# Kernel tuning notes

Hardware: AMD Instinct MI355X
Metric: run time of the kernel (lower is better)

The kernel has to match this reference:

```python
import jax, jax.numpy as jnp
import numpy as np

RADIUS = 3
TEMP = 0.1
EPS = 1e-6


def bilinear_resize(x, oh, ow):
    # Matches torch F.interpolate(mode='bilinear', align_corners=False):
    # half-pixel centers, source coord clamped to >= 0, no antialiasing.
    b, c, h, w = x.shape
    ys = jnp.maximum((jnp.arange(oh, dtype=x.dtype) + 0.5) * (h / oh) - 0.5, 0.0)
    xs = jnp.maximum((jnp.arange(ow, dtype=x.dtype) + 0.5) * (w / ow) - 0.5, 0.0)
    y0f = jnp.floor(ys)
    x0f = jnp.floor(xs)
    wy = (ys - y0f)[:, None]          # [oh,1]
    wx = (xs - x0f)[None, :]          # [1,ow]
    y0 = jnp.clip(y0f, 0, h - 1).astype(jnp.int32)
    y1 = jnp.clip(y0f + 1, 0, h - 1).astype(jnp.int32)
    x0 = jnp.clip(x0f, 0, w - 1).astype(jnp.int32)
    x1 = jnp.clip(x0f + 1, 0, w - 1).astype(jnp.int32)
    r0 = x[:, :, y0, :]
    r1 = x[:, :, y1, :]
    v00 = r0[:, :, :, x0]; v01 = r0[:, :, :, x1]
    v10 = r1[:, :, :, x0]; v11 = r1[:, :, :, x1]
    return (1 - wy) * ((1 - wx) * v00 + wx * v01) + wy * ((1 - wx) * v10 + wx * v11)


def setup_inputs() -> dict:
    key = jax.random.key(0)
    k1, k2, k3 = jax.random.split(key, 3)
    fL = jax.random.normal(k1, (4, 256, 96, 320), dtype=jnp.float32)
    fR = jax.random.normal(k2, (4, 256, 96, 320), dtype=jnp.float32)
    disp_full = jax.random.uniform(k3, (4, 1, 384, 1280), dtype=jnp.float32) * 64.0
    return {"fL": fL, "fR": fR, "disp_full": disp_full}


def reference(fL, fR, disp_full):
    B, C, h4, w4 = fL.shape
    H, W = disp_full.shape[-2], disp_full.shape[-1]
    # quarter-res disparity
    disp0 = bilinear_resize(disp_full, h4, w4) / 4.0            # [B,1,h4,w4]
    # cosine correlation volume over 2*radius+1 horizontal shifts
    nL = fL / jnp.clip(jnp.linalg.norm(fL, axis=1, keepdims=True), EPS)
    nR = fR / jnp.clip(jnp.linalg.norm(fR, axis=1, keepdims=True), EPS)
    sims = [jnp.sum(nL * jnp.roll(nR, d, axis=-1), axis=1)
            for d in range(-RADIUS, RADIUS + 1)]
    # original wraps build_cosine_cost in @torch.no_grad()
    cost = jax.lax.stop_gradient(jnp.stack(sims, axis=1))       # [B,7,h4,w4]
    p = jax.nn.softmax(cost / TEMP, axis=1)
    offsets = jnp.arange(-RADIUS, RADIUS + 1, dtype=fL.dtype).reshape(1, -1, 1, 1)
    delta = jnp.sum(p * offsets, axis=1, keepdims=True)          # [B,1,h4,w4]
    disp_ref = disp0 + delta
    conf = jnp.max(p, axis=1, keepdims=True)
    # laplacian smoothing (smooth=True)
    lap = jnp.array([[0., 1., 0.], [1., -4., 1.], [0., 1., 0.]], dtype=fL.dtype).reshape(1, 1, 3, 3)
    lap_out = jax.lax.conv_general_dilated(disp_ref, lap, (1, 1), [(1, 1), (1, 1)])
    disp_q = disp_ref - 0.2 * lap_out
    disp_full_ref = bilinear_resize(disp_q, H, W) * 4.0
    conf_full = bilinear_resize(conf, H, W)
    return disp_full_ref, conf_full
```

## Files before the change

### kernel.cpp

```cpp
#include <hip/hip_runtime.h>
#include <math.h>

constexpr int B_ = 4, C_ = 256, H4 = 96, W4 = 320, HF = 384, WF = 1280;
constexpr int CHUNKS = 5;
constexpr float EPSV = 1e-6f;
constexpr int LOW = B_ * H4 * W4;
constexpr int FULL = B_ * HF * WF;

__global__ __launch_bounds__(256)
void phase1(const float* __restrict__ fL, const float* __restrict__ fR,
            const float* __restrict__ D, float* __restrict__ dref,
            float* __restrict__ conf)
{
    const int bi = blockIdx.x;
    const int chunk = bi % CHUNKS;
    const int y = (bi / CHUNKS) % H4;
    const int b = bi / (CHUNKS * H4);
    const int tid = threadIdx.x;
    const int wave = tid >> 6;
    const int lane = tid & 63;
    const int x0 = chunk * 64;
    const int x = x0 + lane;

    const size_t chanStride = (size_t)H4 * W4;
    const size_t rowBase = (((size_t)b * C_) * H4 + y) * W4;

    int hx = x, hslot = 0;
    const bool isHalo = (lane < 6);
    if (lane < 3)      { hx = x0 - 3 + lane;        if (hx < 0)   hx += W4; hslot = lane; }
    else if (lane < 6) { hx = x0 + 64 + (lane - 3); if (hx >= W4) hx -= W4; hslot = 64 + lane; }

    float dot[7] = {0.f,0.f,0.f,0.f,0.f,0.f,0.f};
    float ssL = 0.f, ssR = 0.f, ssH = 0.f;

    __shared__ float4 stage4[4][72];
    float4* const sw = stage4[wave];

    const float* pLb = fL + rowBase + (size_t)(wave * 64) * chanStride;
    const float* pRb = fR + rowBase + (size_t)(wave * 64) * chanStride;

    float aa[4], rr[4], hh[4];
    size_t off = 0;
#pragma unroll
    for (int j = 0; j < 4; ++j) {
        aa[j] = pLb[off + x]; rr[j] = pRb[off + x]; hh[j] = pRb[off + hx];
        off += chanStride;
    }

#pragma unroll 4
    for (int it = 0; it < 16; ++it) {
        const float ca0 = aa[0], ca1 = aa[1], ca2 = aa[2], ca3 = aa[3];
        const float4 rq = make_float4(rr[0], rr[1], rr[2], rr[3]);
        const float4 hq = make_float4(hh[0], hh[1], hh[2], hh[3]);

        sw[3 + lane] = rq;
        if (isHalo) sw[hslot] = hq;

        if (it < 15) {
#pragma unroll
            for (int j = 0; j < 4; ++j) {
                aa[j] = pLb[off + x]; rr[j] = pRb[off + x]; hh[j] = pRb[off + hx];
                off += chanStride;
            }
        }

        __builtin_amdgcn_s_waitcnt(0xC07F);

#pragma unroll
        for (int k = 0; k < 7; ++k) {
            const float4 t = sw[lane + k];
            dot[k] += ca0 * t.x + ca1 * t.y + ca2 * t.z + ca3 * t.w;
        }
        ssL += ca0 * ca0 + ca1 * ca1 + ca2 * ca2 + ca3 * ca3;
        ssR += rq.x * rq.x + rq.y * rq.y + rq.z * rq.z + rq.w * rq.w;
        ssH += hq.x * hq.x + hq.y * hq.y + hq.z * hq.z + hq.w * hq.w;
    }

    __shared__ float part[256][11];
    __shared__ float sss[70];
#pragma unroll
    for (int k = 0; k < 7; ++k) part[tid][k] = dot[k];
    part[tid][7] = ssL;
    part[tid][8] = ssR;
    part[tid][9] = ssH;
    __syncthreads();

    float rdot[7], rssL = 0.f;
    if (tid < 64) {
#pragma unroll
        for (int k = 0; k < 7; ++k)
            rdot[k] = part[tid][k] + part[tid + 64][k] + part[tid + 128][k] + part[tid + 192][k];
        rssL = part[tid][7] + part[tid + 64][7] + part[tid + 128][7] + part[tid + 192][7];
        float rssR = part[tid][8] + part[tid + 64][8] + part[tid + 128][8] + part[tid + 192][8];
        sss[3 + tid] = rssR;
        if (tid < 6) {
            float hh2 = part[tid][9] + part[tid + 64][9] + part[tid + 128][9] + part[tid + 192][9];
            if (tid < 3) sss[tid] = hh2;
            else         sss[64 + tid] = hh2;
        }
    }
    __syncthreads();

    if (tid < 64) {
        const float nL = fmaxf(sqrtf(rssL), EPSV);
        float cost[7];
#pragma unroll
        for (int k = 0; k < 7; ++k) {
            float nR = fmaxf(sqrtf(sss[tid + k]), EPSV);
            float s = rdot[k] / (nL * nR);
            cost[6 - k] = s * 10.0f;
        }
        float m = cost[0];
#pragma unroll
        for (int i = 1; i < 7; ++i) m = fmaxf(m, cost[i]);
        float sum = 0.f, dsum = 0.f;
#pragma unroll
        for (int i = 0; i < 7; ++i) {
            float e = __expf(cost[i] - m);
            sum += e;
            dsum += e * (float)(i - 3);
        }
        const float delta = dsum / sum;
        const float cf = 1.0f / sum;

        const int xpix = x0 + tid;
        const int Y0 = 4 * y + 1, X0 = 4 * xpix + 1;
        const size_t dbase = ((size_t)b * HF + Y0) * WF + X0;
        const float s4 = D[dbase] + D[dbase + 1] + D[dbase + WF] + D[dbase + WF + 1];
        const float disp0 = s4 * 0.0625f;

        const size_t o = ((size_t)b * H4 + y) * W4 + xpix;
        dref[o] = disp0 + delta;
        conf[o] = cf;
    }
}

__device__ __forceinline__ float dq_val(const float* __restrict__ dref,
                                        size_t base, int yq, int xq)
{
    size_t i = base + (size_t)yq * W4 + xq;
    float c  = dref[i];
    float up = (yq > 0)      ? dref[i - W4] : 0.f;
    float dn = (yq < H4 - 1) ? dref[i + W4] : 0.f;
    float lf = (xq > 0)      ? dref[i - 1]  : 0.f;
    float rt = (xq < W4 - 1) ? dref[i + 1]  : 0.f;
    return c - 0.2f * (up + dn + lf + rt - 4.f * c);
}

__global__ void phase2(const float* __restrict__ dref, const float* __restrict__ cf,
                       float* __restrict__ out)
{
    int i = blockIdx.x * blockDim.x + threadIdx.x;
    if (i >= FULL) return;
    int X = i % WF;
    int Y = (i / WF) % HF;
    int b = i / (WF * HF);
    float ys = fmaxf((Y + 0.5f) * 0.25f - 0.5f, 0.f);
    float xs = fmaxf((X + 0.5f) * 0.25f - 0.5f, 0.f);
    float y0f = floorf(ys), x0f = floorf(xs);
    float wy = ys - y0f, wx = xs - x0f;
    int y0 = min((int)y0f, H4 - 1);
    int x0 = min((int)x0f, W4 - 1);
    int y1 = min(y0 + 1, H4 - 1);
    int x1 = min(x0 + 1, W4 - 1);
    size_t base = (size_t)b * (H4 * W4);

    float d = (1.f - wy) * ((1.f - wx) * dq_val(dref, base, y0, x0) + wx * dq_val(dref, base, y0, x1))
            +        wy  * ((1.f - wx) * dq_val(dref, base, y1, x0) + wx * dq_val(dref, base, y1, x1));

    size_t i00 = base + (size_t)y0 * W4 + x0;
    size_t i01 = base + (size_t)y0 * W4 + x1;
    size_t i10 = base + (size_t)y1 * W4 + x0;
    size_t i11 = base + (size_t)y1 * W4 + x1;
    float cv = (1.f - wy) * ((1.f - wx) * cf[i00] + wx * cf[i01])
             +        wy  * ((1.f - wx) * cf[i10] + wx * cf[i11]);

    out[i] = 4.0f * d;
    out[(size_t)FULL + i] = cv;
}

extern "C" void kernel_launch(void* const* d_in, const int* in_sizes, int n_in,
                              void* d_out, int out_size, void* d_ws, size_t ws_size,
                              hipStream_t stream)
{
    const float* fL = (const float*)d_in[0];
    const float* fR = (const float*)d_in[1];
    const float* D  = (const float*)d_in[2];
    float* out  = (float*)d_out;
    float* ws   = (float*)d_ws;
    float* dref = ws;
    float* conf = ws + LOW;

    phase1<<<B_ * H4 * CHUNKS, 256, 0, stream>>>(fL, fR, D, dref, conf);
    phase2<<<(FULL + 255) / 256, 256, 0, stream>>>(dref, conf, out);
}
```

Before: 284.8 us.

## Register-tile correlation with float4 loads and shuffle reductions instead of LDS staging

Result: no change. 287.0 us (+0.8%).

```diff
diff --git a/kernel.cpp b/kernel.cpp
--- a/kernel.cpp
+++ b/kernel.cpp
@@ -6,6 +6,32 @@
 constexpr float EPSV = 1e-6f;
 constexpr int LOW = B_ * H4 * W4;
 constexpr int FULL = B_ * HF * WF;
+
+__device__ __forceinline__ void accum_batch(
+    const float4 vL, const float4 wA, const float4 wB, const float4 wC,
+    const bool rsel, float* __restrict__ acc, float* __restrict__ sL,
+    float* __restrict__ sR, float* __restrict__ sH)
+{
+    const float lv[4]  = {vL.x, vL.y, vL.z, vL.w};
+    const float wv[12] = {wA.x, wA.y, wA.z, wA.w,
+                          wB.x, wB.y, wB.z, wB.w,
+                          wC.x, wC.y, wC.z, wC.w};
+#pragma unroll
+    for (int k = 0; k < 7; ++k)
+#pragma unroll
+        for (int p = 0; p < 4; ++p)
+            acc[k * 4 + p] = fmaf(lv[p], wv[p + k + 1], acc[k * 4 + p]);
+#pragma unroll
+    for (int p = 0; p < 4; ++p) {
+        sL[p] = fmaf(lv[p], lv[p], sL[p]);
+        sR[p] = fmaf(wv[4 + p], wv[4 + p], sR[p]);
+    }
+#pragma unroll
+    for (int j = 0; j < 3; ++j) {
+        const float t = rsel ? wv[8 + j] : wv[1 + j];
+        sH[j] = fmaf(t, t, sH[j]);
+    }
+}
 
 __global__ __launch_bounds__(256)
 void phase1(const float* __restrict__ fL, const float* __restrict__ fR,
@@ -19,96 +45,117 @@
     const int tid = threadIdx.x;
     const int wave = tid >> 6;
     const int lane = tid & 63;
+    const int q = lane & 15;
+    const int csub = lane >> 4;
     const int x0 = chunk * 64;
-    const int x = x0 + lane;
+    const int xo = x0 + 4 * q;
 
     const size_t chanStride = (size_t)H4 * W4;
     const size_t rowBase = (((size_t)b * C_) * H4 + y) * W4;
 
-    int hx = x, hslot = 0;
-    const bool isHalo = (lane < 6);
-    if (lane < 3)      { hx = x0 - 3 + lane;        if (hx < 0)   hx += W4; hslot = lane; }
-    else if (lane < 6) { hx = x0 + 64 + (lane - 3); if (hx >= W4) hx -= W4; hslot = 64 + lane; }
-
-    float dot[7] = {0.f,0.f,0.f,0.f,0.f,0.f,0.f};
-    float ssL = 0.f, ssR = 0.f, ssH = 0.f;
-
-    __shared__ float4 stage4[4][72];
-    float4* const sw = stage4[wave];
-
-    const float* pLb = fL + rowBase + (size_t)(wave * 64) * chanStride;
-    const float* pRb = fR + rowBase + (size_t)(wave * 64) * chanStride;
-
-    float aa[4], rr[4], hh[4];
+    int lx = xo - 4; if (lx < 0)   lx += W4;
+    int rx = xo + 4; if (rx >= W4) rx -= W4;
+
+    const int c0 = wave * 64 + csub;
+    const float* pL = fL + rowBase + (size_t)c0 * chanStride;
+    const float* pR = fR + rowBase + (size_t)c0 * chanStride;
+    const size_t step = 4 * chanStride;
+
+    float acc[28];
+#pragma unroll
+    for (int i = 0; i < 28; ++i) acc[i] = 0.f;
+    float sL[4] = {0.f, 0.f, 0.f, 0.f};
+    float sR[4] = {0.f, 0.f, 0.f, 0.f};
+    float sH[3] = {0.f, 0.f, 0.f};
+    const bool rsel = (q == 15);
+
+    float4 vL = *(const float4*)(pL + xo);
+    float4 wA = *(const float4*)(pR + lx);
+    float4 wB = *(const float4*)(pR + xo);
+    float4 wC = *(const float4*)(pR + rx);
+
     size_t off = 0;
-#pragma unroll
-    for (int j = 0; j < 4; ++j) {
-        aa[j] = pLb[off + x]; rr[j] = pRb[off + x]; hh[j] = pRb[off + hx];
-        off += chanStride;
-    }
-
-#pragma unroll 4
     for (int it = 0; it < 16; ++it) {
-        const float ca0 = aa[0], ca1 = aa[1], ca2 = aa[2], ca3 = aa[3];
-        const float4 rq = make_float4(rr[0], rr[1], rr[2], rr[3]);
-        const float4 hq = make_float4(hh[0], hh[1], hh[2], hh[3]);
-
-        sw[3 + lane] = rq;
-        if (isHalo) sw[hslot] = hq;
-
+        const float4 cL = vL, cA = wA, cB = wB, cC = wC;
         if (it < 15) {
-#pragma unroll
-            for (int j = 0; j < 4; ++j) {
-                aa[j] = pLb[off + x]; rr[j] = pRb[off + x]; hh[j] = pRb[off + hx];
-                off += chanStride;
-            }
-        }
-
-        __builtin_amdgcn_s_waitcnt(0xC07F);
-
+            off += step;
+            vL = *(const float4*)(pL + off + xo);
+            wA = *(const float4*)(pR + off + lx);
+            wB = *(const float4*)(pR + off + xo);
+            wC = *(const float4*)(pR + off + rx);
+        }
+        accum_batch(cL, cA, cB, cC, rsel, acc, sL, sR, sH);
+    }
+
+#pragma unroll
+    for (int i = 0; i < 28; ++i) {
+        acc[i] += __shfl_xor(acc[i], 16);
+        acc[i] += __shfl_xor(acc[i], 32);
+    }
+#pragma unroll
+    for (int p = 0; p < 4; ++p) {
+        sL[p] += __shfl_xor(sL[p], 16); sL[p] += __shfl_xor(sL[p], 32);
+        sR[p] += __shfl_xor(sR[p], 16); sR[p] += __shfl_xor(sR[p], 32);
+    }
+#pragma unroll
+    for (int j = 0; j < 3; ++j) {
+        sH[j] += __shfl_xor(sH[j], 16);
+        sH[j] += __shfl_xor(sH[j], 32);
+    }
+
+    __shared__ float rec[4][16][37];
+    __shared__ float hrec[4][2][3];
+    __shared__ float sss[70];
+    if (lane < 16) {
+#pragma unroll
+        for (int i = 0; i < 28; ++i) rec[wave][lane][i] = acc[i];
+#pragma unroll
+        for (int p = 0; p < 4; ++p) {
+            rec[wave][lane][28 + p] = sL[p];
+            rec[wave][lane][32 + p] = sR[p];
+        }
+    }
+    if (lane == 0) {
+#pragma unroll
+        for (int j = 0; j < 3; ++j) hrec[wave][0][j] = sH[j];
+    }
+    if (lane == 15) {
+#pragma unroll
+        for (int j = 0; j < 3; ++j) hrec[wave][1][j] = sH[j];
+    }
+    __syncthreads();
+
+    float D7[7];
+    float rsL = 0.f;
+    if (tid < 64) {
+        const int qq = tid >> 2, pp = tid & 3;
+#pragma unroll
+        for (int k = 0; k < 7; ++k)
+            D7[k] = rec[0][qq][4 * k + pp] + rec[1][qq][4 * k + pp]
+                  + rec[2][qq][4 * k + pp] + rec[3][qq][4 * k + pp];
+        rsL = rec[0][qq][28 + pp] + rec[1][qq][28 + pp]
+            + rec[2][qq][28 + pp] + rec[3][qq][28 + pp];
+        const float rsR = rec[0][qq][32 + pp] + rec[1][qq][32 + pp]
+                        + rec[2][qq][32 + pp] + rec[3][qq][32 + pp];
+        sss[3 + tid] = rsR;
+        if (tid < 3)
+            sss[tid] = hrec[0][0][tid] + hrec[1][0][tid]
+                     + hrec[2][0][tid] + hrec[3][0][tid];
+        if (tid >= 61) {
+            const int j = tid - 61;
+            sss[67 + j] = hrec[0][1][j] + hrec[1][1][j]
+                        + hrec[2][1][j] + hrec[3][1][j];
+        }
+    }
+    __syncthreads();
+
+    if (tid < 64) {
+        const float nLv = fmaxf(sqrtf(rsL), EPSV);
+        float cost[7];
 #pragma unroll
         for (int k = 0; k < 7; ++k) {
-            const float4 t = sw[lane + k];
-            dot[k] += ca0 * t.x + ca1 * t.y + ca2 * t.z + ca3 * t.w;
-        }
-        ssL += ca0 * ca0 + ca1 * ca1 + ca2 * ca2 + ca3 * ca3;
-        ssR += rq.x * rq.x + rq.y * rq.y + rq.z * rq.z + rq.w * rq.w;
-        ssH += hq.x * hq.x + hq.y * hq.y + hq.z * hq.z + hq.w * hq.w;
-    }
-
-    __shared__ float part[256][11];
-    __shared__ float sss[70];
-#pragma unroll
-    for (int k = 0; k < 7; ++k) part[tid][k] = dot[k];
-    part[tid][7] = ssL;
-    part[tid][8] = ssR;
-    part[tid][9] = ssH;
-    __syncthreads();
-
-    float rdot[7], rssL = 0.f;
-    if (tid < 64) {
-#pragma unroll
-        for (int k = 0; k < 7; ++k)
-            rdot[k] = part[tid][k] + part[tid + 64][k] + part[tid + 128][k] + part[tid + 192][k];
-        rssL = part[tid][7] + part[tid + 64][7] + part[tid + 128][7] + part[tid + 192][7];
-        float rssR = part[tid][8] + part[tid + 64][8] + part[tid + 128][8] + part[tid + 192][8];
-        sss[3 + tid] = rssR;
-        if (tid < 6) {
-            float hh2 = part[tid][9] + part[tid + 64][9] + part[tid + 128][9] + part[tid + 192][9];
-            if (tid < 3) sss[tid] = hh2;
-            else         sss[64 + tid] = hh2;
-        }
-    }
-    __syncthreads();
-
-    if (tid < 64) {
-        const float nL = fmaxf(sqrtf(rssL), EPSV);
-        float cost[7];
-#pragma unroll
-        for (int k = 0; k < 7; ++k) {
-            float nR = fmaxf(sqrtf(sss[tid + k]), EPSV);
-            float s = rdot[k] / (nL * nR);
-            cost[6 - k] = s * 10.0f;
+            const float nR = fmaxf(sqrtf(sss[tid + k]), EPSV);
+            cost[6 - k] = (D7[k] / (nLv * nR)) * 10.0f;
         }
         float m = cost[0];
 #pragma unroll
@@ -116,7 +163,7 @@
         float sum = 0.f, dsum = 0.f;
 #pragma unroll
         for (int i = 0; i < 7; ++i) {
-            float e = __expf(cost[i] - m);
+            const float e = __expf(cost[i] - m);
             sum += e;
             dsum += e * (float)(i - 3);
         }
```
